# Kernel tuning notes

Measured on AMD Instinct MI355X. Metric: run time of the kernel, lower is better.

The kernel has to match this reference:

```python
import jax, jax.numpy as jnp
import numpy as np

B, D, E, G, P, H = 8192, 2048, 8, 4, 512, 192
T, DT, TAU, VTH, VRESET = 20, 0.001, 0.02, 0.5, 0.0
DELTA0, KTOP, KROUTE, PREDW = 7.0, 32, 2, 0.1


def setup_inputs() -> dict:
    key = jax.random.key(0)
    ks = jax.random.split(key, 12)
    s = 0.02
    return {
        "query_embedding": jax.random.normal(ks[0], (B, D), jnp.float32),
        "Wg": jax.random.normal(ks[1], (2, E), jnp.float32) * s,
        "bg": jnp.zeros((E,), jnp.float32),
        "Wp": jax.random.normal(ks[2], (2, E), jnp.float32) * s,
        "bp": jnp.zeros((E,), jnp.float32),
        "Wgg": jax.random.normal(ks[3], (2, G), jnp.float32) * s,
        "bgg": jnp.zeros((G,), jnp.float32),
        "W1": jax.random.normal(ks[4], (E, D, P), jnp.float32) * (1.0 / np.sqrt(D)),
        "b1": jnp.zeros((E, P), jnp.float32),
        "W2": jax.random.normal(ks[5], (E, P, D), jnp.float32) * (1.0 / np.sqrt(P)),
        "b2": jnp.zeros((E, D), jnp.float32),
    }


def reference(query_embedding, Wg, bg, Wp, bp, Wgg, bgg, W1, b1, W2, b2):
    x = query_embedding  # [B, D], already embed_dim -> no pad/slice
    dtype = x.dtype

    # --- Phasor bank temporal features on per-row mean ---
    qm = jnp.mean(x, axis=-1)  # [B]
    freqs = DELTA0 * jnp.arange(1, H + 1, dtype=dtype)  # [H]
    ang = qm[:, None] * freqs[None, :]  # [B, H]
    temporal = jnp.concatenate([jnp.cos(ang), jnp.sin(ang)], axis=-1)  # [B, 2H]

    # --- Spiking attention over top-K |x| indices (LIF over T steps) ---
    topk_idx = jax.lax.top_k(jnp.abs(x), KTOP)[1]  # [B, K]
    rows = jnp.arange(B)[:, None]
    I = jnp.zeros((B, D), dtype).at[rows, topk_idx].add(1.0)  # input current [B, vocab=D]

    def lif_step(v, _):
        v = v * (1.0 - DT / TAU) + I
        spike = (v >= VTH).astype(dtype)
        v = jnp.where(spike > 0, VRESET, v)
        return v, spike

    _, spikes = jax.lax.scan(lif_step, jnp.zeros((B, D), dtype), None, length=T)
    attention_gains = jnp.mean(spikes, axis=0)  # [B, D] spike rates

    # --- Bio gating inputs ---
    gate_in = jnp.stack([jnp.mean(temporal, axis=-1), jnp.mean(attention_gains, axis=-1)], axis=-1)  # [B, 2]

    gate_logits = gate_in @ Wg + bg  # [B, E]
    gate_logits = gate_logits - PREDW * (gate_in @ Wp + bp)

    # group routing bias: experts grouped round-robin i % G
    group_logits = gate_in @ Wgg + bgg  # [B, G]
    gmap = jax.nn.one_hot(jnp.arange(E) % G, G, dtype=dtype)  # [E, G]
    gate_logits = gate_logits + group_logits @ gmap.T

    gate_weights = jax.nn.softmax(gate_logits, axis=-1)  # temperature = 1

    # top-k routing + renormalization
    _, tidx = jax.lax.top_k(gate_weights, KROUTE)
    mask = jnp.zeros_like(gate_weights).at[rows, tidx].set(1.0)
    gated = gate_weights * mask
    gate_weights = gated / (jnp.sum(gated, axis=-1, keepdims=True) + 1e-9)

    # --- Dense MLP experts (bottleneck P = hidden // 4) ---
    h = jax.nn.relu(jnp.einsum('bd,edp->ebp', x, W1) + b1[:, None, :])  # [E, B, P]
    expert_out = jnp.einsum('ebp,eph->ebh', h, W2) + b2[:, None, :]  # [E, B, D]

    # gate-weighted combine
    context = jnp.einsum('be,ebh->bh', gate_weights, expert_out)  # [B, D]
    return context
```

## Files before the change

### kernel.cpp

```cpp
#include <hip/hip_runtime.h>
#include <stdint.h>

#define NB 8192
#define ND 2048
#define NE 8
#define NG 4
#define NP 512
#define NH 192

typedef unsigned short u16;
typedef _Float16 half_t;
typedef half_t f16x8 __attribute__((ext_vector_type(8)));
typedef float f32x4 __attribute__((ext_vector_type(4)));

__device__ __forceinline__ void gload16(const void* g, void* l) {
  __builtin_amdgcn_global_load_lds(
      (const __attribute__((address_space(1))) void*)g,
      (__attribute__((address_space(3))) void*)l, 16, 0, 0);
}

__global__ __launch_bounds__(256) void k_convert(
    const float* __restrict__ x, half_t* __restrict__ xh, double* __restrict__ qm)
{
  const int b = blockIdx.x;
  const int t = threadIdx.x;
  const float* xr = x + (size_t)b * ND;
  const float4 v0 = ((const float4*)xr)[t * 2];
  const float4 v1 = ((const float4*)xr)[t * 2 + 1];
  float f[8] = {v0.x, v0.y, v0.z, v0.w, v1.x, v1.y, v1.z, v1.w};
  double s = 0.0;
  __align__(16) half_t hb[8];
#pragma unroll
  for (int i = 0; i < 8; i++) { s += (double)f[i]; hb[i] = (half_t)f[i]; }
  *reinterpret_cast<int4*>(xh + (size_t)b * ND + t * 8) = *reinterpret_cast<const int4*>(hb);

#pragma unroll
  for (int m = 32; m >= 1; m >>= 1) s += __shfl_xor(s, m);
  __shared__ double part[4];
  if ((t & 63) == 0) part[t >> 6] = s;
  __syncthreads();
  if (t == 0) qm[b] = (part[0] + part[1] + part[2] + part[3]) / (double)ND;
}

__global__ __launch_bounds__(256) void k_gate(
    const double* __restrict__ qm,
    const float* __restrict__ Wg, const float* __restrict__ bg,
    const float* __restrict__ Wp, const float* __restrict__ bp,
    const float* __restrict__ Wgg, const float* __restrict__ bgg,
    int* __restrict__ e0a, int* __restrict__ e1a,
    float* __restrict__ w0a, float* __restrict__ w1a)
{
  const int wave = threadIdx.x >> 6;
  const int lane = threadIdx.x & 63;
  const int b = blockIdx.x * 4 + wave;
  const double q = qm[b];

  double part = 0.0;
#pragma unroll
  for (int i = 0; i < 3; i++) {
    int h = lane + i * 64;
    double ang = q * (7.0 * (double)(h + 1));
    part += cos(ang) + sin(ang);
  }
#pragma unroll
  for (int m = 32; m >= 1; m >>= 1) part += __shfl_xor(part, m);
  const double tm = part / (2.0 * (double)NH);
  const double gi1 = 32.0 / 2048.0;

  double lg = -1.0e300;
  if (lane < 8) {
    const int e = lane, g = e & 3;
    lg = tm * (double)Wg[e] + gi1 * (double)Wg[NE + e] + (double)bg[e];
    lg -= 0.1 * (tm * (double)Wp[e] + gi1 * (double)Wp[NE + e] + (double)bp[e]);
    lg += tm * (double)Wgg[g] + gi1 * (double)Wgg[NG + g] + (double)bgg[g];
  }
  double mx = lg;
#pragma unroll
  for (int m = 4; m >= 1; m >>= 1) mx = fmax(mx, __shfl_xor(mx, m));
  double pe = 0.0;
  if (lane < 8) pe = exp(lg - mx);
  double ps = pe;
#pragma unroll
  for (int m = 4; m >= 1; m >>= 1) ps += __shfl_xor(ps, m);

  double lgs[8], pes[8];
#pragma unroll
  for (int e = 0; e < 8; e++) { lgs[e] = __shfl(lg, e); pes[e] = __shfl(pe, e); }

  if (lane == 0) {
    int e0 = 0;
    for (int e = 1; e < NE; e++) if (lgs[e] > lgs[e0]) e0 = e;
    int e1 = (e0 == 0) ? 1 : 0;
    for (int e = 0; e < NE; e++) if (e != e0 && lgs[e] > lgs[e1]) e1 = e;
    const double p0 = pes[e0] / ps;
    const double p1 = pes[e1] / ps;
    const double den = p0 + p1 + 1e-9;
    e0a[b] = e0; e1a[b] = e1;
    w0a[b] = (float)(p0 / den);
    w1a[b] = (float)(p1 / den);
  }
}

#define BUCKET_ROWS 256
__global__ __launch_bounds__(256) void k_bucket(
    const int* __restrict__ e0a, const int* __restrict__ e1a,
    const float* __restrict__ w0a, const float* __restrict__ w1a,
    int* __restrict__ rowl, float* __restrict__ wl, int* __restrict__ cnt)
{
  const int t = threadIdx.x;
  const int r = blockIdx.x * BUCKET_ROWS + t;
  __shared__ int hist[16];
  __shared__ int base[16];
  __shared__ int cursor[16];
  if (t < 16) { hist[t] = 0; cursor[t] = 0; }
  __syncthreads();

  const int e0 = e0a[r], e1 = e1a[r];
  atomicAdd(&hist[e0], 1);
  atomicAdd(&hist[8 + e1], 1);
  __syncthreads();
  if (t < 16) base[t] = atomicAdd(&cnt[t], hist[t]);
  __syncthreads();

  int p0 = atomicAdd(&cursor[e0], 1);
  rowl[e0 * NB + base[e0] + p0] = r;
  wl[e0 * NB + base[e0] + p0] = w0a[r];
  int p1 = atomicAdd(&cursor[8 + e1], 1);
  rowl[(8 + e1) * NB + base[8 + e1] + p1] = r;
  wl[(8 + e1) * NB + base[8 + e1] + p1] = w1a[r];
}

__global__ __launch_bounds__(256) void k_cvt_w(
    const float* __restrict__ W1, const float* __restrict__ W2,
    half_t* __restrict__ w1t, half_t* __restrict__ w2t)
{
  const int which = blockIdx.y;
  const int R = which ? NP : ND;
  const int C = which ? ND : NP;
  const float* src = which ? W2 : W1;
  half_t* dst = which ? w2t : w1t;
  const int tiles_c = C >> 5;
  const int tiles_per_e = (R >> 5) * tiles_c;
  int id = blockIdx.x;
  int e = id / tiles_per_e;
  int rem = id - e * tiles_per_e;
  int tr = rem / tiles_c, tc = rem - tr * tiles_c;
  __shared__ float tile[32][33];
  const int tx = threadIdx.x & 31, ty = threadIdx.x >> 5;
  const float* s = src + (size_t)e * R * C + (size_t)(tr * 32) * C + tc * 32;
#pragma unroll
  for (int i = 0; i < 4; i++)
    tile[ty + i * 8][tx] = s[(size_t)(ty + i * 8) * C + tx];
  __syncthreads();
  half_t* d = dst + (size_t)e * R * C + (size_t)(tc * 32) * R + tr * 32;
#pragma unroll
  for (int i = 0; i < 4; i++)
    d[(size_t)(ty + i * 8) * R + tx] = (half_t)tile[tx][ty + i * 8];
}

__global__ void k_prefix(const int* __restrict__ cnt, int* __restrict__ pbase) {
  if (threadIdx.x == 0 && blockIdx.x == 0) {
    int s = 0;
    for (int i = 0; i < 16; i++) { pbase[i] = s; s += cnt[i]; }
  }
}

__global__ __launch_bounds__(256) void k_gemm1(
    const half_t* __restrict__ xh, const half_t* __restrict__ w1t,
    const float* __restrict__ b1,
    const int* __restrict__ rowl, const int* __restrict__ cnt,
    const int* __restrict__ pbase, half_t* __restrict__ Hbuf)
{
  const int bucket = blockIdx.z;
  const int count = cnt[bucket];
  const int m0 = blockIdx.y * 128;
  if (m0 >= count) return;
  const int e = bucket & 7;
  const int n0 = blockIdx.x * 128;
  const int t = threadIdx.x;

  __shared__ __align__(16) half_t As[128 * 32];
  __shared__ __align__(16) half_t Bs[128 * 32];
  __shared__ int rows_s[128];

  if (t < 128) {
    int mi = m0 + t;
    rows_s[t] = rowl[bucket * NB + (mi < count ? mi : m0)];
  }
  __syncthreads();

  const int w = t >> 6, lane = t & 63;
  const int c0 = w * 128 + lane, c1 = c0 + 64;
  const half_t* gA0 = xh + (size_t)rows_s[c0 >> 2] * ND + (c0 & 3) * 8;
  const half_t* gA1 = xh + (size_t)rows_s[c1 >> 2] * ND + (c1 & 3) * 8;
  const half_t* w1te = w1t + (size_t)e * NP * ND;
  const half_t* gB0 = w1te + (size_t)(n0 + (c0 >> 2)) * ND + (c0 & 3) * 8;
  const half_t* gB1 = w1te + (size_t)(n0 + (c1 >> 2)) * ND + (c1 & 3) * 8;
  half_t* lA0 = As + (w * 128) * 8;
  half_t* lA1 = As + (w * 128 + 64) * 8;
  half_t* lB0 = Bs + (w * 128) * 8;
  half_t* lB1 = Bs + (w * 128 + 64) * 8;

  const int wr = w >> 1, wc = w & 1;
  const int lrow = lane & 15, lk = lane >> 4;

  f32x4 acc[4][4];
#pragma unroll
  for (int i = 0; i < 4; i++)
#pragma unroll
    for (int j = 0; j < 4; j++) {
      acc[i][j][0] = 0.f; acc[i][j][1] = 0.f; acc[i][j][2] = 0.f; acc[i][j][3] = 0.f;
    }

  for (int k0 = 0; k0 < ND; k0 += 32) {
    gload16(gA0 + k0, lA0);
    gload16(gA1 + k0, lA1);
    gload16(gB0 + k0, lB0);
    gload16(gB1 + k0, lB1);
    __syncthreads();
    f16x8 af[4], bf[4];
#pragma unroll
    for (int i = 0; i < 4; i++) {
      af[i] = *reinterpret_cast<const f16x8*>(&As[(wr * 64 + i * 16 + lrow) * 32 + lk * 8]);
      bf[i] = *reinterpret_cast<const f16x8*>(&Bs[(wc * 64 + i * 16 + lrow) * 32 + lk * 8]);
    }
#pragma unroll
    for (int mi = 0; mi < 4; mi++)
#pragma unroll
      for (int ni = 0; ni < 4; ni++)
        acc[mi][ni] = __builtin_amdgcn_mfma_f32_16x16x32_f16(af[mi], bf[ni], acc[mi][ni], 0, 0, 0);
    __syncthreads();
  }

  const int pb = pbase[bucket];
#pragma unroll
  for (int mi = 0; mi < 4; mi++) {
#pragma unroll
    for (int i = 0; i < 4; i++) {
      int lm = wr * 64 + mi * 16 + lk * 4 + i;
      if (m0 + lm < count) {
        size_t prow = (size_t)(pb + m0 + lm) * NP;
#pragma unroll
        for (int ni = 0; ni < 4; ni++) {
          int col = n0 + wc * 64 + ni * 16 + lrow;
          float v = acc[mi][ni][i] + b1[e * NP + col];
          Hbuf[prow + col] = (half_t)(v > 0.f ? v : 0.f);
        }
      }
    }
  }
}

__global__ __launch_bounds__(256) void k_gemm2(
    const half_t* __restrict__ Hbuf, const half_t* __restrict__ w2t,
    const float* __restrict__ b2,
    const int* __restrict__ rowl, const float* __restrict__ wl,
    const int* __restrict__ cnt, const int* __restrict__ pbase,
    float* __restrict__ out, int bucket0, int addmode)
{
  const int bucket = bucket0 + blockIdx.z;
  const int count = cnt[bucket];
  const int m0 = blockIdx.y * 128;
  if (m0 >= count) return;
  const int e = bucket & 7;
  const int n0 = blockIdx.x * 128;
  const int t = threadIdx.x;

  __shared__ __align__(16) half_t As[128 * 32];
  __shared__ __align__(16) half_t Bs[128 * 32];
  __shared__ int rows_s[128];
  __shared__ float ws_s[128];

  if (t < 128) {
    int mi = m0 + t;
    int idx = bucket * NB + (mi < count ? mi : m0);
    rows_s[t] = rowl[idx];
    ws_s[t] = wl[idx];
  }
  __syncthreads();

  const int w = t >> 6, lane = t & 63;
  const int c0 = w * 128 + lane, c1 = c0 + 64;
  const int pb = pbase[bucket];
  const half_t* gA0 = Hbuf + (size_t)(pb + m0 + (c0 >> 2)) * NP + (c0 & 3) * 8;
  const half_t* gA1 = Hbuf + (size_t)(pb + m0 + (c1 >> 2)) * NP + (c1 & 3) * 8;
  const half_t* w2te = w2t + (size_t)e * ND * NP;
  const half_t* gB0 = w2te + (size_t)(n0 + (c0 >> 2)) * NP + (c0 & 3) * 8;
  const half_t* gB1 = w2te + (size_t)(n0 + (c1 >> 2)) * NP + (c1 & 3) * 8;
  half_t* lA0 = As + (w * 128) * 8;
  half_t* lA1 = As + (w * 128 + 64) * 8;
  half_t* lB0 = Bs + (w * 128) * 8;
  half_t* lB1 = Bs + (w * 128 + 64) * 8;

  const int wr = w >> 1, wc = w & 1;
  const int lrow = lane & 15, lk = lane >> 4;

  f32x4 acc[4][4];
#pragma unroll
  for (int i = 0; i < 4; i++)
#pragma unroll
    for (int j = 0; j < 4; j++) {
      acc[i][j][0] = 0.f; acc[i][j][1] = 0.f; acc[i][j][2] = 0.f; acc[i][j][3] = 0.f;
    }

  for (int k0 = 0; k0 < NP; k0 += 32) {
    gload16(gA0 + k0, lA0);
    gload16(gA1 + k0, lA1);
    gload16(gB0 + k0, lB0);
    gload16(gB1 + k0, lB1);
    __syncthreads();
    f16x8 af[4], bf[4];
#pragma unroll
    for (int i = 0; i < 4; i++) {
      af[i] = *reinterpret_cast<const f16x8*>(&As[(wr * 64 + i * 16 + lrow) * 32 + lk * 8]);
      bf[i] = *reinterpret_cast<const f16x8*>(&Bs[(wc * 64 + i * 16 + lrow) * 32 + lk * 8]);
    }
#pragma unroll
    for (int mi = 0; mi < 4; mi++)
#pragma unroll
      for (int ni = 0; ni < 4; ni++)
        acc[mi][ni] = __builtin_amdgcn_mfma_f32_16x16x32_f16(af[mi], bf[ni], acc[mi][ni], 0, 0, 0);
    __syncthreads();
  }

#pragma unroll
  for (int mi = 0; mi < 4; mi++) {
#pragma unroll
    for (int i = 0; i < 4; i++) {
      int lm = wr * 64 + mi * 16 + lk * 4 + i;
      if (m0 + lm < count) {
        int r = rows_s[lm];
        float wgt = ws_s[lm];
        float* orow = out + (size_t)r * ND;
#pragma unroll
        for (int ni = 0; ni < 4; ni++) {
          int col = n0 + wc * 64 + ni * 16 + lrow;
          float v = (acc[mi][ni][i] + b2[e * ND + col]) * wgt;
          if (addmode) orow[col] += v;
          else orow[col] = v;
        }
      }
    }
  }
}

extern "C" void kernel_launch(void* const* d_in, const int* in_sizes, int n_in,
                              void* d_out, int out_size, void* d_ws, size_t ws_size,
                              hipStream_t stream)
{
  const float* x   = (const float*)d_in[0];
  const float* Wg  = (const float*)d_in[1];
  const float* bg  = (const float*)d_in[2];
  const float* Wp  = (const float*)d_in[3];
  const float* bp  = (const float*)d_in[4];
  const float* Wgg = (const float*)d_in[5];
  const float* bgg = (const float*)d_in[6];
  const float* W1  = (const float*)d_in[7];
  const float* b1  = (const float*)d_in[8];
  const float* W2  = (const float*)d_in[9];
  const float* b2  = (const float*)d_in[10];
  float* out = (float*)d_out;

  char* ws = (char*)d_ws;
  const size_t OFF_XH  = 0;
  const size_t OFF_W1T = OFF_XH  + (size_t)NB * ND * 2;
  const size_t OFF_W2T = OFF_W1T + (size_t)NE * NP * ND * 2;
  const size_t OFF_H   = OFF_W2T + (size_t)NE * ND * NP * 2;
  const size_t OFF_ROWL= OFF_H   + (size_t)(2 * NB + 128) * NP * 2;
  const size_t OFF_WL  = OFF_ROWL + (size_t)16 * NB * 4;
  const size_t OFF_CNT = OFF_WL  + (size_t)16 * NB * 4;
  const size_t OFF_PB  = OFF_CNT + 64;
  const size_t OFF_QM  = OFF_PB  + 64;
  const size_t OFF_E0  = OFF_QM  + (size_t)NB * 8;
  const size_t OFF_E1  = OFF_E0  + (size_t)NB * 4;
  const size_t OFF_W0  = OFF_E1  + (size_t)NB * 4;
  const size_t OFF_W1A = OFF_W0  + (size_t)NB * 4;

  half_t* xh   = (half_t*)(ws + OFF_XH);
  half_t* w1t  = (half_t*)(ws + OFF_W1T);
  half_t* w2t  = (half_t*)(ws + OFF_W2T);
  half_t* Hbuf = (half_t*)(ws + OFF_H);
  int*    rowl = (int*)(ws + OFF_ROWL);
  float*  wl   = (float*)(ws + OFF_WL);
  int*    cnt  = (int*)(ws + OFF_CNT);
  int*    pb   = (int*)(ws + OFF_PB);
  double* qm   = (double*)(ws + OFF_QM);
  int*    e0a  = (int*)(ws + OFF_E0);
  int*    e1a  = (int*)(ws + OFF_E1);
  float*  w0a  = (float*)(ws + OFF_W0);
  float*  w1a  = (float*)(ws + OFF_W1A);

  hipMemsetAsync(cnt, 0, 64, stream);
  k_convert<<<NB, 256, 0, stream>>>(x, xh, qm);
  k_cvt_w<<<dim3(8192, 2, 1), 256, 0, stream>>>(W1, W2, w1t, w2t);
  k_gate<<<NB / 4, 256, 0, stream>>>(qm, Wg, bg, Wp, bp, Wgg, bgg, e0a, e1a, w0a, w1a);
  k_bucket<<<NB / BUCKET_ROWS, BUCKET_ROWS, 0, stream>>>(e0a, e1a, w0a, w1a, rowl, wl, cnt);
  k_prefix<<<1, 64, 0, stream>>>(cnt, pb);
  k_gemm1<<<dim3(4, 64, 16), 256, 0, stream>>>(xh, w1t, b1, rowl, cnt, pb, Hbuf);
  k_gemm2<<<dim3(16, 64, 8), 256, 0, stream>>>(Hbuf, w2t, b2, rowl, wl, cnt, pb, out, 0, 0);
  k_gemm2<<<dim3(16, 64, 8), 256, 0, stream>>>(Hbuf, w2t, b2, rowl, wl, cnt, pb, out, 8, 1);
}
```

Measured before the change: 398.7 us.

## Bucket rows by expert pair so gemm2 accumulates both experts in one pass

Rows are also bucketed by their (e0,e1) expert pair. A new gemm2 kernel gathers both experts' hidden rows and runs two K-loops into one accumulator, so each output element is written once. This replaces the two launches, one of which did a read-modify-write of the whole fp32 output. The gate weight is folded into the fp16 hidden activations in gemm1, and both GEMMs walk a compact tile list built in k_prefix instead of a sparse grid of early-exiting blocks. If routing is spread over many pairs, partially filled 128-row tiles may waste work, and scaling before the fp16 cast slightly changes rounding.

```diff
diff --git a/kernel.cpp b/kernel.cpp
--- a/kernel.cpp
+++ b/kernel.cpp
@@ -8,7 +8,6 @@
 #define NP 512
 #define NH 192
 
-typedef unsigned short u16;
 typedef _Float16 half_t;
 typedef half_t f16x8 __attribute__((ext_vector_type(8)));
 typedef float f32x4 __attribute__((ext_vector_type(4)));
@@ -101,33 +100,45 @@
   }
 }
 
-#define BUCKET_ROWS 256
 __global__ __launch_bounds__(256) void k_bucket(
     const int* __restrict__ e0a, const int* __restrict__ e1a,
     const float* __restrict__ w0a, const float* __restrict__ w1a,
-    int* __restrict__ rowl, float* __restrict__ wl, int* __restrict__ cnt)
+    int* __restrict__ rowl, float* __restrict__ wl, int* __restrict__ cnt,
+    int* __restrict__ pos0a, int* __restrict__ pos1a,
+    int* __restrict__ rowlp, int* __restrict__ cntp)
 {
   const int t = threadIdx.x;
-  const int r = blockIdx.x * BUCKET_ROWS + t;
-  __shared__ int hist[16];
-  __shared__ int base[16];
-  __shared__ int cursor[16];
+  const int r = blockIdx.x * 256 + t;
+  __shared__ int hist[16], base[16], cursor[16];
+  __shared__ int histp[64], basep[64], cursorp[64];
   if (t < 16) { hist[t] = 0; cursor[t] = 0; }
+  if (t < 64) { histp[t] = 0; cursorp[t] = 0; }
   __syncthreads();
 
   const int e0 = e0a[r], e1 = e1a[r];
+  const int p = e0 * 8 + e1;
   atomicAdd(&hist[e0], 1);
   atomicAdd(&hist[8 + e1], 1);
+  atomicAdd(&histp[p], 1);
   __syncthreads();
   if (t < 16) base[t] = atomicAdd(&cnt[t], hist[t]);
+  if (t < 64) basep[t] = atomicAdd(&cntp[t], histp[t]);
   __syncthreads();
 
   int p0 = atomicAdd(&cursor[e0], 1);
-  rowl[e0 * NB + base[e0] + p0] = r;
-  wl[e0 * NB + base[e0] + p0] = w0a[r];
+  int idx0 = base[e0] + p0;
+  rowl[e0 * NB + idx0] = r;
+  wl[e0 * NB + idx0] = w0a[r];
+  pos0a[r] = idx0;
+
   int p1 = atomicAdd(&cursor[8 + e1], 1);
-  rowl[(8 + e1) * NB + base[8 + e1] + p1] = r;
-  wl[(8 + e1) * NB + base[8 + e1] + p1] = w1a[r];
+  int idx1 = base[8 + e1] + p1;
+  rowl[(8 + e1) * NB + idx1] = r;
+  wl[(8 + e1) * NB + idx1] = w1a[r];
+  pos1a[r] = idx1;
+
+  int pp = atomicAdd(&cursorp[p], 1);
+  rowlp[p * NB + basep[p] + pp] = r;
 }
 
 __global__ __launch_bounds__(256) void k_cvt_w(
@@ -158,23 +169,38 @@
     d[(size_t)(ty + i * 8) * R + tx] = (half_t)tile[tx][ty + i * 8];
 }
 
-__global__ void k_prefix(const int* __restrict__ cnt, int* __restrict__ pbase) {
+__global__ void k_prefix(const int* __restrict__ cnt, const int* __restrict__ cntp,
+                         int* __restrict__ pbase,
+                         int* __restrict__ i16b, int* __restrict__ i16m, int* __restrict__ n16,
+                         int* __restrict__ ipp, int* __restrict__ ipm, int* __restrict__ np)
+{
   if (threadIdx.x == 0 && blockIdx.x == 0) {
     int s = 0;
     for (int i = 0; i < 16; i++) { pbase[i] = s; s += cnt[i]; }
+    int t = 0;
+    for (int b = 0; b < 16; b++)
+      for (int m0 = 0; m0 < cnt[b]; m0 += 128) { i16b[t] = b; i16m[t] = m0; t++; }
+    *n16 = t;
+    t = 0;
+    for (int p = 0; p < 64; p++)
+      for (int m0 = 0; m0 < cntp[p]; m0 += 128) { ipp[t] = p; ipm[t] = m0; t++; }
+    *np = t;
   }
 }
 
 __global__ __launch_bounds__(256) void k_gemm1(
     const half_t* __restrict__ xh, const half_t* __restrict__ w1t,
     const float* __restrict__ b1,
-    const int* __restrict__ rowl, const int* __restrict__ cnt,
-    const int* __restrict__ pbase, half_t* __restrict__ Hbuf)
-{
-  const int bucket = blockIdx.z;
+    const int* __restrict__ rowl, const float* __restrict__ wl,
+    const int* __restrict__ cnt, const int* __restrict__ pbase,
+    const int* __restrict__ i16b, const int* __restrict__ i16m,
+    const int* __restrict__ n16, half_t* __restrict__ Hbuf)
+{
+  const int wi = blockIdx.y;
+  if (wi >= *n16) return;
+  const int bucket = i16b[wi];
+  const int m0 = i16m[wi];
   const int count = cnt[bucket];
-  const int m0 = blockIdx.y * 128;
-  if (m0 >= count) return;
   const int e = bucket & 7;
   const int n0 = blockIdx.x * 128;
   const int t = threadIdx.x;
@@ -182,10 +208,13 @@
   __shared__ __align__(16) half_t As[128 * 32];
   __shared__ __align__(16) half_t Bs[128 * 32];
   __shared__ int rows_s[128];
+  __shared__ float ws_s[128];
 
   if (t < 128) {
     int mi = m0 + t;
-    rows_s[t] = rowl[bucket * NB + (mi < count ? mi : m0)];
+    int idx = bucket * NB + (mi < count ? mi : m0);
+    rows_s[t] = rowl[idx];
+    ws_s[t] = wl[idx];
   }
   __syncthreads();
 
@@ -240,53 +269,66 @@
       int lm = wr * 64 + mi * 16 + lk * 4 + i;
       if (m0 + lm < count) {
         size_t prow = (size_t)(pb + m0 + lm) * NP;
+        float wcoef = ws_s[lm];
 #pragma unroll
         for (int ni = 0; ni < 4; ni++) {
           int col = n0 + wc * 64 + ni * 16 + lrow;
           float v = acc[mi][ni][i] + b1[e * NP + col];
-          Hbuf[prow + col] = (half_t)(v > 0.f ? v : 0.f);
+          v = v > 0.f ? v : 0.f;
+          Hbuf[prow + col] = (half_t)(v * wcoef);
         }
       }
     }
   }
 }
 
-__global__ __launch_bounds__(256) void k_gemm2(
+__global__ __launch_bounds__(256) void k_gemm2p(
     const half_t* __restrict__ Hbuf, const half_t* __restrict__ w2t,
     const float* __restrict__ b2,
-    const int* __restrict__ rowl, const float* __restrict__ wl,
-    const int* __restrict__ cnt, const int* __restrict__ pbase,
-    float* __restrict__ out, int bucket0, int addmode)
-{
-  const int bucket = bucket0 + blockIdx.z;
-  const int count = cnt[bucket];
-  const int m0 = blockIdx.y * 128;
-  if (m0 >= count) return;
-  const int e = bucket & 7;
+    const int* __restrict__ rowlp, const int* __restrict__ cntp,
+    const int* __restrict__ pbase,
+    const int* __restrict__ pos0a, const int* __restrict__ pos1a,
+    const float* __restrict__ w0a, const float* __restrict__ w1a,
+    const int* __restrict__ ipp, const int* __restrict__ ipm,
+    const int* __restrict__ np, float* __restrict__ out)
+{
+  const int wi = blockIdx.y;
+  if (wi >= *np) return;
+  const int p = ipp[wi];
+  const int m0 = ipm[wi];
+  const int count = cntp[p];
+  const int e0 = p >> 3, e1 = p & 7;
   const int n0 = blockIdx.x * 128;
   const int t = threadIdx.x;
 
   __shared__ __align__(16) half_t As[128 * 32];
   __shared__ __align__(16) half_t Bs[128 * 32];
-  __shared__ int rows_s[128];
-  __shared__ float ws_s[128];
+  __shared__ int h0_s[128], h1_s[128], rs_s[128];
+  __shared__ float w0_s[128], w1_s[128];
 
   if (t < 128) {
     int mi = m0 + t;
-    int idx = bucket * NB + (mi < count ? mi : m0);
-    rows_s[t] = rowl[idx];
-    ws_s[t] = wl[idx];
+    int r = rowlp[p * NB + (mi < count ? mi : m0)];
+    rs_s[t] = r;
+    h0_s[t] = pbase[e0] + pos0a[r];
+    h1_s[t] = pbase[8 + e1] + pos1a[r];
+    w0_s[t] = w0a[r];
+    w1_s[t] = w1a[r];
   }
   __syncthreads();
 
   const int w = t >> 6, lane = t & 63;
   const int c0 = w * 128 + lane, c1 = c0 + 64;
-  const int pb = pbase[bucket];
-  const half_t* gA0 = Hbuf + (size_t)(pb + m0 + (c0 >> 2)) * NP + (c0 & 3) * 8;
-  const half_t* gA1 = Hbuf + (size_t)(pb + m0 + (c1 >> 2)) * NP + (c1 & 3) * 8;
-  const half_t* w2te = w2t + (size_t)e * ND * NP;
-  const half_t* gB0 = w2te + (size_t)(n0 + (c0 >> 2)) * NP + (c0 & 3) * 8;
-  const half_t* gB1 = w2te + (size_t)(n0 + (c1 >> 2)) * NP + (c1 & 3) * 8;
+  const half_t* w2e0 = w2t + (size_t)e0 * ND * NP;
+  const half_t* w2e1 = w2t + (size_t)e1 * ND * NP;
+  const half_t* gB0e0 = w2e0 + (size_t)(n0 + (c0 >> 2)) * NP + (c0 & 3) * 8;
+  const half_t* gB1e0 = w2e0 + (size_t)(n0 + (c1 >> 2)) * NP + (c1 & 3) * 8;
+  const half_t* gB0e1 = w2e1 + (size_t)(n0 + (c0 >> 2)) * NP + (c0 & 3) * 8;
+  const half_t* gB1e1 = w2e1 + (size_t)(n0 + (c1 >> 2)) * NP + (c1 & 3) * 8;
+  const half_t* gA0s0 = Hbuf + (size_t)h0_s[c0 >> 2] * NP + (c0 & 3) * 8;
+  const half_t* gA1s0 = Hbuf + (size_t)h0_s[c1 >> 2] * NP + (c1 & 3) * 8;
+  const half_t* gA0s1 = Hbuf + (size_t)h1_s[c0 >> 2] * NP + (c0 & 3) * 8;
+  const half_t* gA1s1 = Hbuf + (size_t)h1_s[c1 >> 2] * NP + (c1 & 3) * 8;
   half_t* lA0 = As + (w * 128) * 8;
   half_t* lA1 = As + (w * 128 + 64) * 8;
   half_t* lB0 = Bs + (w * 128) * 8;
@@ -304,10 +346,10 @@
     }
 
   for (int k0 = 0; k0 < NP; k0 += 32) {
-    gload16(gA0 + k0, lA0);
-    gload16(gA1 + k0, lA1);
-    gload16(gB0 + k0, lB0);
-    gload16(gB1 + k0, lB1);
+    gload16(gA0s0 + k0, lA0);
+    gload16(gA1s0 + k0, lA1);
+    gload16(gB0e0 + k0, lB0);
+    gload16(gB1e0 + k0, lB1);
     __syncthreads();
     f16x8 af[4], bf[4];
 #pragma unroll
@@ -322,22 +364,46 @@
         acc[mi][ni] = __builtin_amdgcn_mfma_f32_16x16x32_f16(af[mi], bf[ni], acc[mi][ni], 0, 0, 0);
     __syncthreads();
   }
-
+  for (int k0 = 0; k0 < NP; k0 += 32) {
+    gload16(gA0s1 + k0, lA0);
+    gload16(gA1s1 + k0, lA1);
+    gload16(gB0e1 + k0, lB0);
+    gload16(gB1e1 + k0, lB1);
+    __syncthreads();
+    f16x8 af[4], bf[4];
+#pragma unroll
+    for (int i = 0; i < 4; i++) {
+      af[i] = *reinterpret_cast<const f16x8*>(&As[(wr * 64 + i * 16 + lrow) * 32 + lk * 8]);
+      bf[i] = *reinterpret_cast<const f16x8*>(&Bs[(wc * 64 + i * 16 + lrow) * 32 + lk * 8]);
+    }
+#pragma unroll
+    for (int mi = 0; mi < 4; mi++)
+#pragma unroll
+      for (int ni = 0; ni < 4; ni++)
+        acc[mi][ni] = __builtin_amdgcn_mfma_f32_16x16x32_f16(af[mi], bf[ni], acc[mi][ni], 0, 0, 0);
+    __syncthreads();
+  }
+
+  float b20[4], b21[4];
+#pragma unroll
+  for (int ni = 0; ni < 4; ni++) {
+    int col = n0 + wc * 64 + ni * 16 + lrow;
+    b20[ni] = b2[e0 * ND + col];
+    b21[ni] = b2[e1 * ND + col];
+  }
 #pragma unroll
   for (int mi = 0; mi < 4; mi++) {
 #pragma unroll
     for (int i = 0; i < 4; i++) {
       int lm = wr * 64 + mi * 16 + lk * 4 + i;
       if (m0 + lm < count) {
-        int r = rows_s[lm];
-        float wgt = ws_s[lm];
+        int r = rs_s[lm];
+        float wb0 = w0_s[lm], wb1 = w1_s[lm];
         float* orow = out + (size_t)r * ND;
 #pragma unroll
         for (int ni = 0; ni < 4; ni++) {
           int col = n0 + wc * 64 + ni * 16 + lrow;
-          float v = (acc[mi][ni][i] + b2[e * ND + col]) * wgt;
-          if (addmode) orow[col] += v;
-          else orow[col] = v;
+          orow[col] = acc[mi][ni][i] + wb0 * b20[ni] + wb1 * b21[ni];
         }
       }
     }
@@ -362,19 +428,30 @@
   float* out = (float*)d_out;
 
   char* ws = (char*)d_ws;
-  const size_t OFF_XH  = 0;
-  const size_t OFF_W1T = OFF_XH  + (size_t)NB * ND * 2;
-  const size_t OFF_W2T = OFF_W1T + (size_t)NE * NP * ND * 2;
-  const size_t OFF_H   = OFF_W2T + (size_t)NE * ND * NP * 2;
-  const size_t OFF_ROWL= OFF_H   + (size_t)(2 * NB + 128) * NP * 2;
-  const size_t OFF_WL  = OFF_ROWL + (size_t)16 * NB * 4;
-  const size_t OFF_CNT = OFF_WL  + (size_t)16 * NB * 4;
-  const size_t OFF_PB  = OFF_CNT + 64;
-  const size_t OFF_QM  = OFF_PB  + 64;
-  const size_t OFF_E0  = OFF_QM  + (size_t)NB * 8;
-  const size_t OFF_E1  = OFF_E0  + (size_t)NB * 4;
-  const size_t OFF_W0  = OFF_E1  + (size_t)NB * 4;
-  const size_t OFF_W1A = OFF_W0  + (size_t)NB * 4;
+  size_t off = 0;
+  const size_t OFF_XH   = off; off += (size_t)NB * ND * 2;
+  const size_t OFF_W1T  = off; off += (size_t)NE * NP * ND * 2;
+  const size_t OFF_W2T  = off; off += (size_t)NE * ND * NP * 2;
+  const size_t OFF_H    = off; off += (size_t)(2 * NB + 128) * NP * 2;
+  const size_t OFF_ROWL = off; off += (size_t)16 * NB * 4;
+  const size_t OFF_WL   = off; off += (size_t)16 * NB * 4;
+  const size_t OFF_ROWLP= off; off += (size_t)64 * NB * 4;
+  const size_t OFF_CNT  = off; off += 64;
+  const size_t OFF_CNTP = off; off += 256;
+  const size_t OFF_PB   = off; off += 64;
+  const size_t OFF_QM   = off; off += (size_t)NB * 8;
+  const size_t OFF_E0   = off; off += (size_t)NB * 4;
+  const size_t OFF_E1   = off; off += (size_t)NB * 4;
+  const size_t OFF_W0   = off; off += (size_t)NB * 4;
+  const size_t OFF_W1A  = off; off += (size_t)NB * 4;
+  const size_t OFF_POS0 = off; off += (size_t)NB * 4;
+  const size_t OFF_POS1 = off; off += (size_t)NB * 4;
+  const size_t OFF_I16B = off; off += 1024;
+  const size_t OFF_I16M = off; off += 1024;
+  const size_t OFF_N16  = off; off += 64;
+  const size_t OFF_IPP  = off; off += 1024;
+  const size_t OFF_IPM  = off; off += 1024;
+  const size_t OFF_NP   = off; off += 64;
 
   half_t* xh   = (half_t*)(ws + OFF_XH);
   half_t* w1t  = (half_t*)(ws + OFF_W1T);
@@ -382,21 +459,33 @@
   half_t* Hbuf = (half_t*)(ws + OFF_H);
   int*    rowl = (int*)(ws + OFF_ROWL);
   float*  wl   = (float*)(ws + OFF_WL);
+  int*    rowlp= (int*)(ws + OFF_ROWLP);
   int*    cnt  = (int*)(ws + OFF_CNT);
+  int*    cntp = (int*)(ws + OFF_CNTP);
   int*    pb   = (int*)(ws + OFF_PB);
   double* qm   = (double*)(ws + OFF_QM);
   int*    e0a  = (int*)(ws + OFF_E0);
   int*    e1a  = (int*)(ws + OFF_E1);
   float*  w0a  = (float*)(ws + OFF_W0);
   float*  w1a  = (float*)(ws + OFF_W1A);
-
-  hipMemsetAsync(cnt, 0, 64, stream);
+  int*    pos0a= (int*)(ws + OFF_POS0);
+  int*    pos1a= (int*)(ws + OFF_POS1);
+  int*    i16b = (int*)(ws + OFF_I16B);
+  int*    i16m = (int*)(ws + OFF_I16M);
+  int*    n16  = (int*)(ws + OFF_N16);
+  int*    ipp  = (int*)(ws + OFF_IPP);
+  int*    ipm  = (int*)(ws + OFF_IPM);
+  int*    np   = (int*)(ws + OFF_NP);
+
+  hipMemsetAsync(cnt, 0, 64 + 256, stream);
   k_convert<<<NB, 256, 0, stream>>>(x, xh, qm);
   k_cvt_w<<<dim3(8192, 2, 1), 256, 0, stream>>>(W1, W2, w1t, w2t);
   k_gate<<<NB / 4, 256, 0, stream>>>(qm, Wg, bg, Wp, bp, Wgg, bgg, e0a, e1a, w0a, w1a);
-  k_bucket<<<NB / BUCKET_ROWS, BUCKET_ROWS, 0, stream>>>(e0a, e1a, w0a, w1a, rowl, wl, cnt);
-  k_prefix<<<1, 64, 0, stream>>>(cnt, pb);
-  k_gemm1<<<dim3(4, 64, 16), 256, 0, stream>>>(xh, w1t, b1, rowl, cnt, pb, Hbuf);
-  k_gemm2<<<dim3(16, 64, 8), 256, 0, stream>>>(Hbuf, w2t, b2, rowl, wl, cnt, pb, out, 0, 0);
-  k_gemm2<<<dim3(16, 64, 8), 256, 0, stream>>>(Hbuf, w2t, b2, rowl, wl, cnt, pb, out, 8, 1);
-}
+  k_bucket<<<NB / 256, 256, 0, stream>>>(e0a, e1a, w0a, w1a, rowl, wl, cnt,
+                                         pos0a, pos1a, rowlp, cntp);
+  k_prefix<<<1, 64, 0, stream>>>(cnt, cntp, pb, i16b, i16m, n16, ipp, ipm, np);
+  k_gemm1<<<dim3(4, 144, 1), 256, 0, stream>>>(xh, w1t, b1, rowl, wl, cnt, pb,
+                                               i16b, i16m, n16, Hbuf);
+  k_gemm2p<<<dim3(16, 128, 1), 256, 0, stream>>>(Hbuf, w2t, b2, rowlp, cntp, pb,
+                                                 pos0a, pos1a, w0a, w1a, ipp, ipm, np, out);
+}
```

Result: faster. 355.4 us (-10.9%).
